# Kernel tuning notes

Hardware: AMD Instinct MI355X
Metric: run time of the kernel (lower is better)

## Reference

```python
import jax, jax.numpy as jnp
import numpy as np

NB_KNN = (10, 20)   # list of k values (nb_knn)
S = 1.0             # smoothing s (= T)
NUM_CLASSES = 19
N_TRAIN = 16384
N_QUERY = 4096
D_FEAT = 128


def setup_inputs() -> dict:
    key = jax.random.key(0)
    k1, k2, k3 = jax.random.split(key, 3)
    features = jax.random.normal(k1, (N_QUERY, D_FEAT), dtype=jnp.float32)
    train_features = jax.random.normal(k2, (N_TRAIN, D_FEAT), dtype=jnp.float32)
    train_labels = jax.random.randint(k3, (N_TRAIN, NUM_CLASSES), 0, 2, dtype=jnp.int32)
    return {"features": features, "train_features": train_features, "train_labels": train_labels}


def _sq_dists(a, b):
    # squared euclidean distances [Na, Nb]; monotone in euclidean -> same kNN
    return jnp.sum(a * a, -1)[:, None] + jnp.sum(b * b, -1)[None, :] - 2.0 * (a @ b.T)


def reference(features, train_features, train_labels):
    """MLkNN (Zhang & Zhou) as in skmultilearn, for each k in NB_KNN.
    Returns stacked posterior probabilities: [len(NB_KNN), B, C]."""
    max_k = max(NB_KNN)
    n = train_features.shape[0]
    y = train_labels.astype(jnp.float32)  # [N, C]

    # kNN of every train point among train points (self included, as sklearn does
    # when querying the fit set) and kNN of every query among train points.
    d_tt = _sq_dists(train_features, train_features)   # [N, N]
    _, nbr_t = jax.lax.top_k(-d_tt, max_k)             # [N, max_k] sorted by distance
    d_qt = _sq_dists(features, train_features)         # [B, N]
    _, nbr_q = jax.lax.top_k(-d_qt, max_k)             # [B, max_k]

    # priors: P(H1_j) = (s + count_j) / (2s + N)
    prior_true = (S + y.sum(0)) / (2.0 * S + n)        # [C]
    prior_false = 1.0 - prior_true

    cidx = jnp.arange(NUM_CLASSES)[None, :]
    outs = []
    for k in NB_KNN:  # small fixed set of k values (structural loop)
        # delta_j = #neighbors carrying label j, in [0, k]
        deltas_t = jnp.take(train_labels, nbr_t[:, :k], axis=0).sum(1)  # [N, C]
        dh = jax.nn.one_hot(deltas_t, k + 1, dtype=jnp.float32)         # [N, C, k+1]
        c1 = jnp.einsum('nc,ncd->cd', y, dh)        # counts among positives
        c0 = jnp.einsum('nc,ncd->cd', 1.0 - y, dh)  # counts among negatives
        cond_t = (S + c1) / (S * (k + 1) + c1.sum(1, keepdims=True))  # P(delta|H1) [C,k+1]
        cond_f = (S + c0) / (S * (k + 1) + c0.sum(1, keepdims=True))  # P(delta|H0)

        deltas_q = jnp.take(train_labels, nbr_q[:, :k], axis=0).sum(1)  # [B, C]
        pt = prior_true * cond_t[cidx, deltas_q]   # [B, C]
        pf = prior_false * cond_f[cidx, deltas_q]
        outs.append(pt / (pt + pf))                # posterior P(H1|delta)
    return jnp.stack(outs, 0)  # [num_k, B, C]
```

## Files before the change

kernel.cpp:

```cpp
#include <hip/hip_runtime.h>
#include <cstdint>
#include <cstddef>

#define NTR 16384
#define NQR 4096
#define NROW 20480
#define DF  128
#define NCL 19

typedef unsigned short u16;
typedef unsigned int u32;
typedef __attribute__((ext_vector_type(8))) short bf16x8;
typedef __attribute__((ext_vector_type(16))) float f32x16;

#define OFF_RN    (size_t)0
#define OFF_QEXT  (size_t)81920
#define OFF_CEXT  (size_t)5980160
#define OFF_FSN   (size_t)10698752
#define OFF_NBRT  (size_t)18563072
#define OFF_NBRQ  (size_t)19873792
#define OFF_HIST  (size_t)20201472
#define OFF_COND  (size_t)20211200
#define OFF_PRIOR (size_t)20220928
#define WS_NEEDED (size_t)20221008

__device__ __forceinline__ float mulr(float a, float b) {
  float m = a * b;
  asm volatile("" : "+v"(m));
  return m;
}

__device__ __forceinline__ u16 bf16_rne(float x) {
  union { float f; unsigned u; } v; v.f = x;
  unsigned r = (v.u + 0x7fffu + ((v.u >> 16) & 1u)) >> 16;
  return (u16)r;
}
__device__ __forceinline__ float bf16_f32(u16 h) {
  union { unsigned u; float f; } v; v.u = ((unsigned)h) << 16;
  return v.f;
}

__device__ __forceinline__ void gload_lds16(const void* g, void* lds) {
  __builtin_amdgcn_global_load_lds(
      (const __attribute__((address_space(1))) unsigned int*)g,
      (__attribute__((address_space(3))) unsigned int*)lds, 16, 0, 0);
}

__global__ __launch_bounds__(256) void norms_kernel(const float* __restrict__ train,
                                                    const float* __restrict__ feat,
                                                    float* __restrict__ rn) {
  int i = blockIdx.x * 256 + threadIdx.x;
  const float* src = (i < NTR) ? (train + (size_t)i * DF) : (feat + (size_t)(i - NTR) * DF);
  float s = 0.0f;
  for (int k = 0; k < DF; ++k) {
    float x = src[k];
    s = s + mulr(x, x);
  }
  rn[i] = s;
}

__global__ __launch_bounds__(256) void ext_kernel(const float* __restrict__ train,
                                                  const float* __restrict__ feat,
                                                  const float* __restrict__ rn,
                                                  u16* __restrict__ qext,
                                                  u16* __restrict__ cext) {
  int row = blockIdx.x * 2 + (threadIdx.x >> 7);
  int k = threadIdx.x & 127;
  const float* srcp = (row < NTR) ? (train + (size_t)row * DF) : (feat + (size_t)(row - NTR) * DF);
  float x = srcp[k];
  u16 b = bf16_rne(x);
  qext[(size_t)row * 144 + k] = b;
  if (row < NTR) cext[(size_t)row * 144 + k] = (u16)(b ^ 0x8000u);
  if (k < 16) {
    qext[(size_t)row * 144 + 128 + k] = (k < 2) ? (u16)0x3F80 : (u16)0;
    if (row < NTR) {
      float hbf = 0.5f * rn[row] + 256.0f;
      u16 hi = bf16_rne(hbf);
      u16 lo = bf16_rne(hbf - bf16_f32(hi));
      cext[(size_t)row * 144 + 128 + k] = (k == 0) ? hi : ((k == 1) ? lo : (u16)0);
    }
  }
}

__global__ __launch_bounds__(256, 4) void filter_kernel(const u16* __restrict__ qext,
                                                        const u16* __restrict__ cext,
                                                        u16* __restrict__ fsn) {
  __shared__ __align__(16) char smem[36864];
  const int bid = blockIdx.x;
  const int slice = bid & 3, rowblk = bid >> 2;
  const int grow0 = rowblk * 64;
  const int cslice0 = slice * 4096;
  const int tid = threadIdx.x;
  const int wave = tid >> 6, lane = tid & 63;
  const int wq = wave >> 1, wc = wave & 1;
  const int l31 = lane & 31, h = lane >> 5;
  const char* qb = (const char*)qext;
  const char* cbg = (const char*)cext;

  bf16x8 qf[9];
  const int qrow = grow0 + wq * 32 + l31;
#pragma unroll
  for (int ks = 0; ks < 8; ++ks)
    qf[ks] = *(const bf16x8*)(qb + (size_t)qrow * 288 + ks * 32 + h * 16);
  qf[8] = *(const bf16x8*)(qb + (size_t)qrow * 288 + 256 + h * 16);

  u32 sd[16];
#pragma unroll
  for (int t = 0; t < 16; ++t) sd[t] = 0x7F7FFFFFu;
  float th_f = __uint_as_float(0x7F7FF000u);

  const char* srcA[4];
#pragma unroll
  for (int j = 0; j < 4; ++j) {
    int I = wave + 4 * j;
    int G = I * 64 + lane;
    int r = G >> 4, g = G & 15;
    srcA[j] = cbg + (size_t)(cslice0 + r) * 288 + ((g << 4) ^ ((r & 7) << 4));
  }
  const char* srcH = nullptr;
  if (wave < 2) {
    int GG = wave * 64 + lane;
    int r = GG >> 1, half = GG & 1;
    srcH = cbg + (size_t)(cslice0 + r) * 288 + 256 + half * 16;
  }

  auto STAGE = [&](int buf) {
    char* cb = smem + buf * 16384;
    char* hb = smem + 32768 + buf * 2048;
#pragma unroll
    for (int j = 0; j < 4; ++j) {
      int I = wave + 4 * j;
      gload_lds16(srcA[j], cb + I * 1024);
      srcA[j] += 64 * 288;
    }
    if (wave < 2) {
      gload_lds16(srcH, hb + wave * 1024);
      srcH += 64 * 288;
    }
  };

  STAGE(0);
  __syncthreads();

  const int crow = wc * 32 + l31;
  for (int nt = 0; nt < 64; ++nt) {
    const int cur = nt & 1;
    if (nt < 63) STAGE(cur ^ 1);

    const char* cbp = smem + cur * 16384 + crow * 256;
    const char* hbp = smem + 32768 + cur * 2048 + crow * 32 + h * 16;
    f32x16 acc = {0.f,0.f,0.f,0.f,0.f,0.f,0.f,0.f,0.f,0.f,0.f,0.f,0.f,0.f,0.f,0.f};
#pragma unroll
    for (int ks = 0; ks < 8; ++ks) {
      bf16x8 cf = *(const bf16x8*)(cbp + ((ks * 32 + h * 16) ^ ((crow & 7) << 4)));
      acc = __builtin_amdgcn_mfma_f32_32x32x16_bf16(cf, qf[ks], acc, 0, 0, 0);
    }
    {
      bf16x8 cf = *(const bf16x8*)hbp;
      acc = __builtin_amdgcn_mfma_f32_32x32x16_bf16(cf, qf[8], acc, 0, 0, 0);
    }

    float f01 = fminf(acc[0], acc[1]),   f23 = fminf(acc[2], acc[3]);
    float f45 = fminf(acc[4], acc[5]),   f67 = fminf(acc[6], acc[7]);
    float f89 = fminf(acc[8], acc[9]),   fab = fminf(acc[10], acc[11]);
    float fcd = fminf(acc[12], acc[13]), fef = fminf(acc[14], acc[15]);
    float tmin_f = fminf(fminf(fminf(f01, f23), fminf(f45, f67)),
                         fminf(fminf(f89, fab), fminf(fcd, fef)));
    if (tmin_f < th_f) {
      const u32 cb_idx = (u32)(nt * 64 + wc * 32 + 4 * h);
      u32 tk[16];
#pragma unroll
      for (int j = 0; j < 16; ++j) {
        u32 off = (u32)((j & 3) + 8 * (j >> 2));
        tk[j] = (__float_as_uint(acc[j]) & 0xFFFFF000u) + cb_idx + off;
      }
#pragma unroll
      for (int k = 2; k <= 16; k <<= 1)
#pragma unroll
        for (int j = k >> 1; j > 0; j >>= 1)
#pragma unroll
          for (int i = 0; i < 16; ++i) {
            int l = i ^ j;
            if (l > i) {
              bool asc = ((i & k) == 0);
              u32 a = tk[i], b = tk[l];
              u32 lo = a < b ? a : b, hi = a < b ? b : a;
              tk[i] = asc ? lo : hi;
              tk[l] = asc ? hi : lo;
            }
          }
      u32 m[16];
#pragma unroll
      for (int i = 0; i < 16; ++i) {
        u32 a = sd[i], b = tk[15 - i];
        m[i] = a < b ? a : b;
      }
#pragma unroll
      for (int j = 8; j > 0; j >>= 1)
#pragma unroll
        for (int i = 0; i < 16; ++i) {
          int l = i ^ j;
          if (l > i) {
            u32 a = m[i], b = m[l];
            m[i] = a < b ? a : b;
            m[l] = a < b ? b : a;
          }
        }
#pragma unroll
      for (int i = 0; i < 16; ++i) sd[i] = m[i];
      th_f = __uint_as_float(sd[15] & 0xFFFFF000u);
    }
    __syncthreads();
  }

  u32* md = (u32*)smem;
  {
    int b = tid * 16;
#pragma unroll
    for (int t = 0; t < 16; ++t) md[b + t] = sd[t];
  }
  __syncthreads();
  if (tid < 64) {
    const int r = tid;
    const int rwq = r >> 5, rl = r & 31;
    const u32* L[4];
#pragma unroll
    for (int wcc = 0; wcc < 2; ++wcc)
#pragma unroll
      for (int hh = 0; hh < 2; ++hh)
        L[wcc * 2 + hh] = md + (size_t)((rwq * 2 + wcc) * 64 + hh * 32 + rl) * 16;
    int p0 = 0, p1 = 0, p2 = 0, p3 = 0;
    size_t ob = (size_t)(grow0 + r) * 96 + (size_t)slice * 24;
    for (int t = 0; t < 24; ++t) {
      u32 k0 = (p0 < 16) ? L[0][p0] : 0xFFFFFFFFu;
      u32 k1 = (p1 < 16) ? L[1][p1] : 0xFFFFFFFFu;
      u32 k2 = (p2 < 16) ? L[2][p2] : 0xFFFFFFFFu;
      u32 k3 = (p3 < 16) ? L[3][p3] : 0xFFFFFFFFu;
      bool a01 = k0 <= k1; u32 kA = a01 ? k0 : k1;
      bool a23 = k2 <= k3; u32 kB = a23 ? k2 : k3;
      bool ab = kA <= kB;  u32 km = ab ? kA : kB;
      fsn[ob + t] = (u16)(cslice0 + (km & 0xFFFu));
      int win = ab ? (a01 ? 0 : 1) : (a23 ? 2 : 3);
      p0 += (win == 0); p1 += (win == 1); p2 += (win == 2); p3 += (win == 3);
    }
  }
}

__global__ __launch_bounds__(192) void rescore_kernel(const float* __restrict__ train,
                                                      const float* __restrict__ feat,
                                                      const float* __restrict__ rn,
                                                      const u16* __restrict__ fsn,
                                                      int* __restrict__ nbrt,
                                                      int* __restrict__ nbrq) {
  __shared__ __align__(16) float rowf[2][DF];
  __shared__ __align__(16) float sc[2][96];
  __shared__ __align__(16) int sidx[2][96];
  const int tid = threadIdx.x;
  const int sub = (tid >= 96) ? 1 : 0;
  const int t = tid - sub * 96;
  const int row = blockIdx.x * 2 + sub;
  const float* src = (row < NTR) ? (train + (size_t)row * DF) : (feat + (size_t)(row - NTR) * DF);
  for (int i = t; i < DF; i += 96) rowf[sub][i] = src[i];
  __syncthreads();
  {
    int ci = (int)fsn[(size_t)row * 96 + t];
    if (ci >= NTR) ci = NTR - 1;
    const float* tv = train + (size_t)ci * DF;
    float4 b0 = *(const float4*)(tv + 0);
    float4 b1 = *(const float4*)(tv + 4);
    float4 b2 = *(const float4*)(tv + 8);
    float4 b3 = *(const float4*)(tv + 12);
    float s = 0.0f;
#pragma unroll
    for (int ch = 0; ch < 8; ++ch) {
      float4 n0, n1, n2, n3;
      if (ch < 7) {
        const float* nx = tv + (ch + 1) * 16;
        n0 = *(const float4*)(nx + 0);
        n1 = *(const float4*)(nx + 4);
        n2 = *(const float4*)(nx + 8);
        n3 = *(const float4*)(nx + 12);
      }
      float4 q0 = *(const float4*)&rowf[sub][ch * 16 + 0];
      float4 q1 = *(const float4*)&rowf[sub][ch * 16 + 4];
      float4 q2 = *(const float4*)&rowf[sub][ch * 16 + 8];
      float4 q3 = *(const float4*)&rowf[sub][ch * 16 + 12];
      s = s + mulr(q0.x, b0.x); s = s + mulr(q0.y, b0.y);
      s = s + mulr(q0.z, b0.z); s = s + mulr(q0.w, b0.w);
      s = s + mulr(q1.x, b1.x); s = s + mulr(q1.y, b1.y);
      s = s + mulr(q1.z, b1.z); s = s + mulr(q1.w, b1.w);
      s = s + mulr(q2.x, b2.x); s = s + mulr(q2.y, b2.y);
      s = s + mulr(q2.z, b2.z); s = s + mulr(q2.w, b2.w);
      s = s + mulr(q3.x, b3.x); s = s + mulr(q3.y, b3.y);
      s = s + mulr(q3.z, b3.z); s = s + mulr(q3.w, b3.w);
      if (ch < 7) { b0 = n0; b1 = n1; b2 = n2; b3 = n3; }
    }
    float t1 = rn[row] + rn[ci];
    sc[sub][t] = t1 - 2.0f * s;
    sidx[sub][t] = ci;
  }
  __syncthreads();
  {
    float dm = sc[sub][t];
    int im = sidx[sub][t];
    int rank = 0;
#pragma unroll 4
    for (int i = 0; i < 96; i += 4) {
      float4 d4 = *(const float4*)&sc[sub][i];
      int4 i4 = *(const int4*)&sidx[sub][i];
      rank += (d4.x < dm || (d4.x == dm && i4.x < im));
      rank += (d4.y < dm || (d4.y == dm && i4.y < im));
      rank += (d4.z < dm || (d4.z == dm && i4.z < im));
      rank += (d4.w < dm || (d4.w == dm && i4.w < im));
    }
    if (rank < 20) {
      int* outp = (row < NTR) ? (nbrt + (size_t)row * 20) : (nbrq + (size_t)(row - NTR) * 20);
      outp[rank] = im;
    }
  }
}

__global__ __launch_bounds__(256) void hist_kernel(const int* __restrict__ labels,
                                                   const int* __restrict__ nbrt,
                                                   int* __restrict__ ghist) {
  __shared__ int h[2432];
  int tid = threadIdx.x;
  for (int i = tid; i < 2432; i += 256) h[i] = 0;
  __syncthreads();
  int row = blockIdx.x * 256 + tid;
  int nb[20];
#pragma unroll
  for (int j = 0; j < 20; ++j) nb[j] = nbrt[(size_t)row * 20 + j];
  int cnt[NCL];
#pragma unroll
  for (int c = 0; c < NCL; ++c) cnt[c] = 0;
#pragma unroll
  for (int j = 0; j < 10; ++j) {
    const int* lr = labels + (size_t)nb[j] * NCL;
#pragma unroll
    for (int c = 0; c < NCL; ++c) cnt[c] += lr[c];
  }
  const int* myl = labels + (size_t)row * NCL;
  int my[NCL];
#pragma unroll
  for (int c = 0; c < NCL; ++c) my[c] = myl[c];
#pragma unroll
  for (int c = 0; c < NCL; ++c)
    atomicAdd(&h[((0 * 2 + my[c]) * NCL + c) * 32 + cnt[c]], 1);
#pragma unroll
  for (int j = 10; j < 20; ++j) {
    const int* lr = labels + (size_t)nb[j] * NCL;
#pragma unroll
    for (int c = 0; c < NCL; ++c) cnt[c] += lr[c];
  }
#pragma unroll
  for (int c = 0; c < NCL; ++c)
    atomicAdd(&h[((1 * 2 + my[c]) * NCL + c) * 32 + cnt[c]], 1);
  __syncthreads();
  for (int i = tid; i < 2432; i += 256) {
    int v = h[i];
    if (v) atomicAdd(&ghist[i], v);
  }
}

__global__ __launch_bounds__(256) void prep_kernel(const int* __restrict__ ghist,
                                                   float* __restrict__ cond,
                                                   float* __restrict__ prior) {
  __shared__ int cpos[NCL];
  int tid = threadIdx.x;
  if (tid < NCL) {
    int s = 0;
    for (int d = 0; d < 32; ++d) s += ghist[((0 * 2 + 1) * NCL + tid) * 32 + d];
    cpos[tid] = s;
    prior[tid] = (1.0f + (float)s) / (2.0f + (float)NTR);
  }
  __syncthreads();
  for (int i = tid; i < 2432; i += 256) {
    int cc = (i >> 5) % NCL;
    int pos = ((i >> 5) / NCL) & 1;
    int ki = i / (2 * NCL * 32);
    int k = ki ? 20 : 10;
    float num = 1.0f + (float)ghist[i];
    float den = (float)(k + 1) + (float)(pos ? cpos[cc] : (NTR - cpos[cc]));
    cond[i] = num / den;
  }
}

__global__ __launch_bounds__(256) void out_kernel(const int* __restrict__ labels,
                                                  const int* __restrict__ nbrq,
                                                  const float* __restrict__ cond,
                                                  const float* __restrict__ prior,
                                                  float* __restrict__ out) {
  int q = blockIdx.x * 256 + threadIdx.x;
  int nb[20];
#pragma unroll
  for (int j = 0; j < 20; ++j) nb[j] = nbrq[(size_t)q * 20 + j];
  int cnt[NCL], d10[NCL];
#pragma unroll
  for (int c = 0; c < NCL; ++c) cnt[c] = 0;
#pragma unroll
  for (int j = 0; j < 10; ++j) {
    const int* lr = labels + (size_t)nb[j] * NCL;
#pragma unroll
    for (int c = 0; c < NCL; ++c) cnt[c] += lr[c];
  }
#pragma unroll
  for (int c = 0; c < NCL; ++c) d10[c] = cnt[c];
#pragma unroll
  for (int j = 10; j < 20; ++j) {
    const int* lr = labels + (size_t)nb[j] * NCL;
#pragma unroll
    for (int c = 0; c < NCL; ++c) cnt[c] += lr[c];
  }
#pragma unroll
  for (int ki = 0; ki < 2; ++ki) {
#pragma unroll
    for (int c = 0; c < NCL; ++c) {
      int delta = ki ? cnt[c] : d10[c];
      float pr = prior[c];
      float pt = pr * cond[((ki * 2 + 1) * NCL + c) * 32 + delta];
      float pf = (1.0f - pr) * cond[((ki * 2 + 0) * NCL + c) * 32 + delta];
      out[((size_t)ki * NQR + q) * NCL + c] = pt / (pt + pf);
    }
  }
}

extern "C" void kernel_launch(void* const* d_in, const int* in_sizes, int n_in,
                              void* d_out, int out_size, void* d_ws, size_t ws_size,
                              hipStream_t stream) {
  const float* feat = (const float*)d_in[0];
  const float* train = (const float*)d_in[1];
  const int* labels = (const int*)d_in[2];
  float* out = (float*)d_out;
  if (ws_size < WS_NEEDED) return;
  char* w = (char*)d_ws;
  float* rn = (float*)(w + OFF_RN);
  u16* qext = (u16*)(w + OFF_QEXT);
  u16* cext = (u16*)(w + OFF_CEXT);
  u16* fsn = (u16*)(w + OFF_FSN);
  int* nbrt = (int*)(w + OFF_NBRT);
  int* nbrq = (int*)(w + OFF_NBRQ);
  int* ghist = (int*)(w + OFF_HIST);
  float* cond = (float*)(w + OFF_COND);
  float* prior = (float*)(w + OFF_PRIOR);

  hipMemsetAsync(ghist, 0, 2432 * 4, stream);
  norms_kernel<<<80, 256, 0, stream>>>(train, feat, rn);
  ext_kernel<<<10240, 256, 0, stream>>>(train, feat, rn, qext, cext);
  filter_kernel<<<1280, 256, 0, stream>>>(qext, cext, fsn);
  rescore_kernel<<<10240, 192, 0, stream>>>(train, feat, rn, fsn, nbrt, nbrq);
  hist_kernel<<<64, 256, 0, stream>>>(labels, nbrt, ghist);
  prep_kernel<<<1, 256, 0, stream>>>(ghist, cond, prior);
  out_kernel<<<16, 256, 0, stream>>>(labels, nbrq, cond, prior, out);
}
```

Baseline: 427.2 us.

## Stage candidate tiles through registers into a single LDS buffer to raise occupancy

The filter kernel swaps its double-buffered direct global-to-LDS copy of candidate tiles for a single 16 KB LDS buffer. The next tile is prefetched into registers during compute and written to LDS between two barriers. The constant query extension fragment is built in registers instead of loaded, and the merge works on sd in place. Shared memory drops from 36 KB to 20 KB and launch bounds rise to 5 blocks per SU, in exchange for an extra barrier per tile and more register pressure from the prefetch buffers.

Result: slower. 710.5 us (+66.3%).

```diff
diff --git a/kernel.cpp b/kernel.cpp
--- a/kernel.cpp
+++ b/kernel.cpp
@@ -82,10 +82,10 @@
   }
 }
 
-__global__ __launch_bounds__(256, 4) void filter_kernel(const u16* __restrict__ qext,
+__global__ __launch_bounds__(256, 5) void filter_kernel(const u16* __restrict__ qext,
                                                         const u16* __restrict__ cext,
                                                         u16* __restrict__ fsn) {
-  __shared__ __align__(16) char smem[36864];
+  __shared__ __align__(16) char smem[20480];
   const int bid = blockIdx.x;
   const int slice = bid & 3, rowblk = bid >> 2;
   const int grow0 = rowblk * 64;
@@ -97,12 +97,13 @@
   const char* qb = (const char*)qext;
   const char* cbg = (const char*)cext;
 
-  bf16x8 qf[9];
+  bf16x8 qf[8];
   const int qrow = grow0 + wq * 32 + l31;
 #pragma unroll
   for (int ks = 0; ks < 8; ++ks)
     qf[ks] = *(const bf16x8*)(qb + (size_t)qrow * 288 + ks * 32 + h * 16);
-  qf[8] = *(const bf16x8*)(qb + (size_t)qrow * 288 + 256 + h * 16);
+  bf16x8 qf8 = (bf16x8){0, 0, 0, 0, 0, 0, 0, 0};
+  if (h == 0) { qf8[0] = (short)0x3F80; qf8[1] = (short)0x3F80; }
 
   u32 sd[16];
 #pragma unroll
@@ -124,31 +125,39 @@
     srcH = cbg + (size_t)(cslice0 + r) * 288 + 256 + half * 16;
   }
 
-  auto STAGE = [&](int buf) {
-    char* cb = smem + buf * 16384;
-    char* hb = smem + 32768 + buf * 2048;
+  float4 vA[4];
+  auto LOADC = [&]() {
+#pragma unroll
+    for (int j = 0; j < 4; ++j) {
+      vA[j] = *(const float4*)srcA[j];
+      srcA[j] += 64 * 288;
+    }
+  };
+  auto WRITEC = [&]() {
 #pragma unroll
     for (int j = 0; j < 4; ++j) {
       int I = wave + 4 * j;
-      gload_lds16(srcA[j], cb + I * 1024);
-      srcA[j] += 64 * 288;
-    }
+      *(float4*)(smem + I * 1024 + lane * 16) = vA[j];
+    }
+  };
+  auto STAGEH = [&](int buf) {
     if (wave < 2) {
-      gload_lds16(srcH, hb + wave * 1024);
+      gload_lds16(srcH, smem + 16384 + buf * 2048 + wave * 1024);
       srcH += 64 * 288;
     }
   };
 
-  STAGE(0);
+  LOADC();
+  STAGEH(0);
+  WRITEC();
   __syncthreads();
 
   const int crow = wc * 32 + l31;
   for (int nt = 0; nt < 64; ++nt) {
-    const int cur = nt & 1;
-    if (nt < 63) STAGE(cur ^ 1);
-
-    const char* cbp = smem + cur * 16384 + crow * 256;
-    const char* hbp = smem + 32768 + cur * 2048 + crow * 32 + h * 16;
+    if (nt < 63) { LOADC(); STAGEH((nt + 1) & 1); }
+
+    const char* cbp = smem + crow * 256;
+    const char* hbp = smem + 16384 + (nt & 1) * 2048 + crow * 32 + h * 16;
     f32x16 acc = {0.f,0.f,0.f,0.f,0.f,0.f,0.f,0.f,0.f,0.f,0.f,0.f,0.f,0.f,0.f,0.f};
 #pragma unroll
     for (int ks = 0; ks < 8; ++ks) {
@@ -157,7 +166,7 @@
     }
     {
       bf16x8 cf = *(const bf16x8*)hbp;
-      acc = __builtin_amdgcn_mfma_f32_32x32x16_bf16(cf, qf[8], acc, 0, 0, 0);
+      acc = __builtin_amdgcn_mfma_f32_32x32x16_bf16(cf, qf8, acc, 0, 0, 0);
     }
 
     float f01 = fminf(acc[0], acc[1]),   f23 = fminf(acc[2], acc[3]);
@@ -189,11 +198,10 @@
               tk[l] = asc ? hi : lo;
             }
           }
-      u32 m[16];
 #pragma unroll
       for (int i = 0; i < 16; ++i) {
-        u32 a = sd[i], b = tk[15 - i];
-        m[i] = a < b ? a : b;
+        u32 b = tk[15 - i];
+        sd[i] = sd[i] < b ? sd[i] : b;
       }
 #pragma unroll
       for (int j = 8; j > 0; j >>= 1)
@@ -201,15 +209,16 @@
         for (int i = 0; i < 16; ++i) {
           int l = i ^ j;
           if (l > i) {
-            u32 a = m[i], b = m[l];
-            m[i] = a < b ? a : b;
-            m[l] = a < b ? b : a;
+            u32 a = sd[i], b = sd[l];
+            sd[i] = a < b ? a : b;
+            sd[l] = a < b ? b : a;
           }
         }
-#pragma unroll
-      for (int i = 0; i < 16; ++i) sd[i] = m[i];
       th_f = __uint_as_float(sd[15] & 0xFFFFF000u);
     }
+
+    __syncthreads();
+    if (nt < 63) WRITEC();
     __syncthreads();
   }
 
```

## Halve filter column slices to two, shrinking candidate set to 48 per row

Applied to the files above, without the earlier changes.

The filter kernel now splits the train columns into 2 slices of 8192 instead of 4 of 4096. Each block loops 128 tiles, and the packed-key index field grows to 13 bits, which costs one bit of distance precision. Each row now emits 48 candidates instead of 96, so the rescore kernel processes 4 rows per block with 48 threads each and uses a deeper 4-chunk prefetch of train vectors. The aim is to halve the exact rescoring work and the candidate traffic, at the cost of longer serial filter blocks, fewer blocks (640), and coarser key quantization that may reduce recall.

Result: faster. 413.5 us (-3.2%).

```diff
diff --git a/kernel.cpp b/kernel.cpp
--- a/kernel.cpp
+++ b/kernel.cpp
@@ -87,9 +87,9 @@
                                                         u16* __restrict__ fsn) {
   __shared__ __align__(16) char smem[36864];
   const int bid = blockIdx.x;
-  const int slice = bid & 3, rowblk = bid >> 2;
+  const int slice = bid & 1, rowblk = bid >> 1;
   const int grow0 = rowblk * 64;
-  const int cslice0 = slice * 4096;
+  const int cslice0 = slice * 8192;
   const int tid = threadIdx.x;
   const int wave = tid >> 6, lane = tid & 63;
   const int wq = wave >> 1, wc = wave & 1;
@@ -107,7 +107,7 @@
   u32 sd[16];
 #pragma unroll
   for (int t = 0; t < 16; ++t) sd[t] = 0x7F7FFFFFu;
-  float th_f = __uint_as_float(0x7F7FF000u);
+  float th_f = __uint_as_float(0x7F7FE000u);
 
   const char* srcA[4];
 #pragma unroll
@@ -126,7 +126,6 @@
 
   auto STAGE = [&](int buf) {
     char* cb = smem + buf * 16384;
-    char* hb = smem + 32768 + buf * 2048;
 #pragma unroll
     for (int j = 0; j < 4; ++j) {
       int I = wave + 4 * j;
@@ -134,7 +133,7 @@
       srcA[j] += 64 * 288;
     }
     if (wave < 2) {
-      gload_lds16(srcH, hb + wave * 1024);
+      gload_lds16(srcH, smem + 32768 + buf * 2048 + wave * 1024);
       srcH += 64 * 288;
     }
   };
@@ -143,9 +142,9 @@
   __syncthreads();
 
   const int crow = wc * 32 + l31;
-  for (int nt = 0; nt < 64; ++nt) {
+  for (int nt = 0; nt < 128; ++nt) {
     const int cur = nt & 1;
-    if (nt < 63) STAGE(cur ^ 1);
+    if (nt < 127) STAGE(cur ^ 1);
 
     const char* cbp = smem + cur * 16384 + crow * 256;
     const char* hbp = smem + 32768 + cur * 2048 + crow * 32 + h * 16;
@@ -172,7 +171,7 @@
 #pragma unroll
       for (int j = 0; j < 16; ++j) {
         u32 off = (u32)((j & 3) + 8 * (j >> 2));
-        tk[j] = (__float_as_uint(acc[j]) & 0xFFFFF000u) + cb_idx + off;
+        tk[j] = (__float_as_uint(acc[j]) & 0xFFFFE000u) + cb_idx + off;
       }
 #pragma unroll
       for (int k = 2; k <= 16; k <<= 1)
@@ -189,11 +188,10 @@
               tk[l] = asc ? hi : lo;
             }
           }
-      u32 m[16];
 #pragma unroll
       for (int i = 0; i < 16; ++i) {
-        u32 a = sd[i], b = tk[15 - i];
-        m[i] = a < b ? a : b;
+        u32 b = tk[15 - i];
+        sd[i] = sd[i] < b ? sd[i] : b;
       }
 #pragma unroll
       for (int j = 8; j > 0; j >>= 1)
@@ -201,14 +199,12 @@
         for (int i = 0; i < 16; ++i) {
           int l = i ^ j;
           if (l > i) {
-            u32 a = m[i], b = m[l];
-            m[i] = a < b ? a : b;
-            m[l] = a < b ? b : a;
+            u32 a = sd[i], b = sd[l];
+            sd[i] = a < b ? a : b;
+            sd[l] = a < b ? b : a;
           }
         }
-#pragma unroll
-      for (int i = 0; i < 16; ++i) sd[i] = m[i];
-      th_f = __uint_as_float(sd[15] & 0xFFFFF000u);
+      th_f = __uint_as_float(sd[15] & 0xFFFFE000u);
     }
     __syncthreads();
   }
@@ -230,7 +226,7 @@
       for (int hh = 0; hh < 2; ++hh)
         L[wcc * 2 + hh] = md + (size_t)((rwq * 2 + wcc) * 64 + hh * 32 + rl) * 16;
     int p0 = 0, p1 = 0, p2 = 0, p3 = 0;
-    size_t ob = (size_t)(grow0 + r) * 96 + (size_t)slice * 24;
+    size_t ob = (size_t)(grow0 + r) * 48 + (size_t)slice * 24;
     for (int t = 0; t < 24; ++t) {
       u32 k0 = (p0 < 16) ? L[0][p0] : 0xFFFFFFFFu;
       u32 k1 = (p1 < 16) ? L[1][p1] : 0xFFFFFFFFu;
@@ -239,7 +235,7 @@
       bool a01 = k0 <= k1; u32 kA = a01 ? k0 : k1;
       bool a23 = k2 <= k3; u32 kB = a23 ? k2 : k3;
       bool ab = kA <= kB;  u32 km = ab ? kA : kB;
-      fsn[ob + t] = (u16)(cslice0 + (km & 0xFFFu));
+      fsn[ob + t] = (u16)(cslice0 + (km & 0x1FFFu));
       int win = ab ? (a01 ? 0 : 1) : (a23 ? 2 : 3);
       p0 += (win == 0); p1 += (win == 1); p2 += (win == 2); p3 += (win == 3);
     }
@@ -252,39 +248,39 @@
                                                       const u16* __restrict__ fsn,
                                                       int* __restrict__ nbrt,
                                                       int* __restrict__ nbrq) {
-  __shared__ __align__(16) float rowf[2][DF];
-  __shared__ __align__(16) float sc[2][96];
-  __shared__ __align__(16) int sidx[2][96];
+  __shared__ __align__(16) float rowf[4][132];
+  __shared__ __align__(16) float sc[4][52];
+  __shared__ __align__(16) int sidx[4][52];
   const int tid = threadIdx.x;
-  const int sub = (tid >= 96) ? 1 : 0;
-  const int t = tid - sub * 96;
-  const int row = blockIdx.x * 2 + sub;
+  const int sub = tid / 48;
+  const int t = tid - sub * 48;
+  const int row = blockIdx.x * 4 + sub;
   const float* src = (row < NTR) ? (train + (size_t)row * DF) : (feat + (size_t)(row - NTR) * DF);
-  for (int i = t; i < DF; i += 96) rowf[sub][i] = src[i];
+  for (int i = t; i < DF; i += 48) rowf[sub][i] = src[i];
   __syncthreads();
   {
-    int ci = (int)fsn[(size_t)row * 96 + t];
+    int ci = (int)fsn[(size_t)row * 48 + t];
     if (ci >= NTR) ci = NTR - 1;
     const float* tv = train + (size_t)ci * DF;
-    float4 b0 = *(const float4*)(tv + 0);
-    float4 b1 = *(const float4*)(tv + 4);
-    float4 b2 = *(const float4*)(tv + 8);
-    float4 b3 = *(const float4*)(tv + 12);
+    float4 B0[4], B1[4], B2[4], B3[4];
+#pragma unroll
+    for (int p = 0; p < 4; ++p) {
+      const float* cp = tv + p * 16;
+      float4* Bp = (p == 0) ? B0 : (p == 1) ? B1 : (p == 2) ? B2 : B3;
+      Bp[0] = *(const float4*)(cp + 0);
+      Bp[1] = *(const float4*)(cp + 4);
+      Bp[2] = *(const float4*)(cp + 8);
+      Bp[3] = *(const float4*)(cp + 12);
+    }
     float s = 0.0f;
 #pragma unroll
     for (int ch = 0; ch < 8; ++ch) {
-      float4 n0, n1, n2, n3;
-      if (ch < 7) {
-        const float* nx = tv + (ch + 1) * 16;
-        n0 = *(const float4*)(nx + 0);
-        n1 = *(const float4*)(nx + 4);
-        n2 = *(const float4*)(nx + 8);
-        n3 = *(const float4*)(nx + 12);
-      }
+      float4* B = ((ch & 3) == 0) ? B0 : ((ch & 3) == 1) ? B1 : ((ch & 3) == 2) ? B2 : B3;
       float4 q0 = *(const float4*)&rowf[sub][ch * 16 + 0];
       float4 q1 = *(const float4*)&rowf[sub][ch * 16 + 4];
       float4 q2 = *(const float4*)&rowf[sub][ch * 16 + 8];
       float4 q3 = *(const float4*)&rowf[sub][ch * 16 + 12];
+      float4 b0 = B[0], b1 = B[1], b2 = B[2], b3 = B[3];
       s = s + mulr(q0.x, b0.x); s = s + mulr(q0.y, b0.y);
       s = s + mulr(q0.z, b0.z); s = s + mulr(q0.w, b0.w);
       s = s + mulr(q1.x, b1.x); s = s + mulr(q1.y, b1.y);
@@ -293,7 +289,13 @@
       s = s + mulr(q2.z, b2.z); s = s + mulr(q2.w, b2.w);
       s = s + mulr(q3.x, b3.x); s = s + mulr(q3.y, b3.y);
       s = s + mulr(q3.z, b3.z); s = s + mulr(q3.w, b3.w);
-      if (ch < 7) { b0 = n0; b1 = n1; b2 = n2; b3 = n3; }
+      if (ch < 4) {
+        const float* cp = tv + (ch + 4) * 16;
+        B[0] = *(const float4*)(cp + 0);
+        B[1] = *(const float4*)(cp + 4);
+        B[2] = *(const float4*)(cp + 8);
+        B[3] = *(const float4*)(cp + 12);
+      }
     }
     float t1 = rn[row] + rn[ci];
     sc[sub][t] = t1 - 2.0f * s;
@@ -304,8 +306,8 @@
     float dm = sc[sub][t];
     int im = sidx[sub][t];
     int rank = 0;
-#pragma unroll 4
-    for (int i = 0; i < 96; i += 4) {
+#pragma unroll 3
+    for (int i = 0; i < 48; i += 4) {
       float4 d4 = *(const float4*)&sc[sub][i];
       int4 i4 = *(const int4*)&sidx[sub][i];
       rank += (d4.x < dm || (d4.x == dm && i4.x < im));
@@ -447,8 +449,8 @@
   hipMemsetAsync(ghist, 0, 2432 * 4, stream);
   norms_kernel<<<80, 256, 0, stream>>>(train, feat, rn);
   ext_kernel<<<10240, 256, 0, stream>>>(train, feat, rn, qext, cext);
-  filter_kernel<<<1280, 256, 0, stream>>>(qext, cext, fsn);
-  rescore_kernel<<<10240, 192, 0, stream>>>(train, feat, rn, fsn, nbrt, nbrq);
+  filter_kernel<<<640, 256, 0, stream>>>(qext, cext, fsn);
+  rescore_kernel<<<5120, 192, 0, stream>>>(train, feat, rn, fsn, nbrt, nbrq);
   hist_kernel<<<64, 256, 0, stream>>>(labels, nbrt, ghist);
   prep_kernel<<<1, 256, 0, stream>>>(ghist, cond, prior);
   out_kernel<<<16, 256, 0, stream>>>(labels, nbrq, cond, prior, out);
```
